# Performance work log

Hardware: AMD Instinct MI355X
Metric: run time of the kernel (lower is better)

The kernel has to match this reference:

```python
import jax, jax.numpy as jnp
import numpy as np

# physical / init constants (from DPINeuron.__init__ with default 1e-12 currents)
I0 = 5e-13
UT = 0.025
KAPPA = (0.75 + 0.66) / 2  # 0.705
CMEM, CAMPA, CSHUNT = 3e-12, 2e-12, 2e-12
ITAU_MEM = 1e-12
IGAIN_MEM = 1e-12
ITAU_AMPA = 1e-12
IGAIN_AMPA = 1e-12
ITH = 1e-12
IPFB_TH = 1e-12
IPFB_NORM = 1e-12
REFP = 0.0
DT = 0.001
TAU_MEM = UT / KAPPA * CMEM / ITAU_MEM
TAU_AMPA = UT / KAPPA * CAMPA / ITAU_AMPA
TAU_SHUNT = UT / KAPPA * CSHUNT / ITAU_AMPA
SLOPE = 25.0  # fast_sigmoid surrogate slope

@jax.custom_vjp
def ste_round(x):
    return jnp.round(x)

def _round_fwd(x):
    return jnp.round(x), None

def _round_bwd(_, g):
    return (g,)  # straight-through estimator

ste_round.defvjp(_round_fwd, _round_bwd)

@jax.custom_vjp
def fast_sigmoid(x):
    return (x > 0).astype(x.dtype)

def _fs_fwd(x):
    return (x > 0).astype(x.dtype), x

def _fs_bwd(x, g):
    return (g / (SLOPE * jnp.abs(x) + 1.0) ** 2,)

fast_sigmoid.defvjp(_fs_fwd, _fs_bwd)

B, N_IN, N_OUT = 4096, 2048, 2048

def setup_inputs() -> dict:
    key = jax.random.key(0)
    k1, = jax.random.split(key, 1)
    X = (jax.random.uniform(k1, (B, N_IN), dtype=jnp.float32) < 0.1).astype(jnp.float32)  # sparse input spikes
    return {
        "X": X,
        "W_ampa": jnp.ones((N_OUT, N_IN), jnp.float32),   # init.constant_(1.0)
        "W_shunt": jnp.ones((N_OUT, N_IN), jnp.float32),
        "Imem": jnp.full((B, N_OUT), I0, jnp.float32),    # initialize(): zeros + I0
        "Iampa": jnp.full((B, N_OUT), I0, jnp.float32),
        "Ishunt": jnp.full((B, N_OUT), I0, jnp.float32),
        "refractory": jnp.zeros((B, N_OUT), jnp.float32),
        "Idc": jnp.float32(1e-12),
        "Iw_ampa": jnp.float32(1e-12),
        "Iw_shunt": jnp.float32(1e-12),
        "alpha": jnp.float32(IGAIN_MEM / ITAU_MEM),       # 1.0
        "beta": jnp.float32(1.0 + I0 / ITAU_MEM),         # 1.5
    }

def reference(X, W_ampa, W_shunt, Imem, Iampa, Ishunt, refractory,
              Idc, Iw_ampa, Iw_shunt, alpha, beta):
    Iahp = I0
    Inmda = I0
    # synapse projections with STE-rounded weights: [B, n_out]
    numSynAmpa = jnp.einsum('bi,oi->bo', X, ste_round(W_ampa))
    numSynShunt = jnp.einsum('bi,oi->bo', X, ste_round(W_shunt))

    dIampa = -Iampa / TAU_AMPA
    Iampa = Iampa + (IGAIN_AMPA / ITAU_AMPA) * Iw_ampa * numSynAmpa
    dIshunt = -Ishunt / TAU_SHUNT
    Ishunt = Ishunt + (IGAIN_AMPA / ITAU_AMPA) * Iw_shunt * numSynShunt

    Iin = Idc + Iampa + Inmda - Ishunt
    Iin = Iin * (refractory <= 0)
    Iin = jnp.maximum(Iin, I0)

    Ifb = (I0 ** (1.0 / (KAPPA + 1.0))) * Imem ** (KAPPA / (KAPPA + 1.0)) \
          / (1.0 + jnp.exp(-IPFB_NORM * (Imem - IPFB_TH)))
    f_imem = Ifb / ITAU_MEM * (Imem + IGAIN_MEM)
    dImem = (alpha * (Iin - ITAU_MEM - Iahp) - beta * Imem
             + jax.lax.stop_gradient(f_imem)) / (TAU_MEM * (1.0 + IGAIN_MEM / Imem))
    Imem = jnp.maximum(Imem + dImem * DT, I0)

    # note: original code applies dIshunt decay to Iampa (kept faithful)
    Iampa = jnp.maximum(Iampa + dIampa * DT, I0)
    Iampa = jnp.maximum(Iampa + dIshunt * DT, I0)

    spike = fast_sigmoid(Imem - ITH)
    Imem = (1.0 - spike) * Imem + spike * I0
    refractory = jnp.maximum(refractory - DT, 0.0)
    refractory = (1.0 - spike) * refractory + spike * REFP
    return spike, Imem, Iampa, Ishunt, refractory
```

## Files before the change

### kernel.cpp

```cpp
#include <hip/hip_runtime.h>
#include <cmath>

#ifndef __has_builtin
#define __has_builtin(x) 0
#endif

#define B_DIM 4096
#define K_DIM 2048
#define N_DIM 2048

#define BM 128
#define BN 128
#define BK 64

typedef __attribute__((ext_vector_type(4))) float f32x4;
typedef __attribute__((ext_vector_type(4))) int i32x4;
typedef __attribute__((ext_vector_type(16))) signed char i8x16;


__device__ __forceinline__ signed char f2i8(float f) {
    int t = __float2int_rn(f);
    t = t < -127 ? -127 : (t > 127 ? 127 : t);
    return (signed char)t;
}

__device__ __forceinline__ void gl2lds16(const void* g, void* l) {
#if __has_builtin(__builtin_amdgcn_global_load_lds)
    __builtin_amdgcn_global_load_lds((__attribute__((address_space(1))) void*)g,
                                     (__attribute__((address_space(3))) void*)l,
                                     16, 0, 0);
#else
    *(uint4*)l = *(const uint4*)g;
#endif
}

#define VMWAIT_(n) asm volatile("s_waitcnt vmcnt(" #n ")" ::: "memory")
#define VMWAIT(n)  VMWAIT_(n)
#define FENCE      asm volatile("" ::: "memory")
#define SBARRIER   do { FENCE; __builtin_amdgcn_s_barrier(); FENCE; } while (0)


__global__ void cast_x_kernel(const float* __restrict__ X,
                              signed char* __restrict__ Xb) {
    size_t i = ((size_t)blockIdx.x * 256 + threadIdx.x) * 16;
    i8x16 o;
#pragma unroll
    for (int j = 0; j < 16; j += 4) {
        f32x4 a = *(const f32x4*)(X + i + j);
        o[j]     = f2i8(a[0]);
        o[j + 1] = f2i8(a[1]);
        o[j + 2] = f2i8(a[2]);
        o[j + 3] = f2i8(a[3]);
    }
    *(i8x16*)(Xb + i) = o;
}

__global__ void cast_w_kernel(const float* __restrict__ Wa,
                              const float* __restrict__ Ws,
                              signed char* __restrict__ Wab,
                              signed char* __restrict__ Wsb) {
    size_t i = ((size_t)blockIdx.x * 256 + threadIdx.x) * 16;
    i8x16 oa, os;
#pragma unroll
    for (int j = 0; j < 16; j += 4) {
        f32x4 a = *(const f32x4*)(Wa + i + j);
        f32x4 s = *(const f32x4*)(Ws + i + j);
        oa[j]     = f2i8(a[0]); oa[j + 1] = f2i8(a[1]);
        oa[j + 2] = f2i8(a[2]); oa[j + 3] = f2i8(a[3]);
        os[j]     = f2i8(s[0]); os[j + 1] = f2i8(s[1]);
        os[j + 2] = f2i8(s[2]); os[j + 3] = f2i8(s[3]);
    }
    *(i8x16*)(Wab + i) = oa;
    *(i8x16*)(Wsb + i) = os;
}


#define RS 132

__device__ __forceinline__ void stage_tile(int tt, int bufIdx, int tid, int m0, int n0,
                                           unsigned char* smem,
                                           const signed char* __restrict__ Xb,
                                           const signed char* __restrict__ Wab,
                                           const signed char* __restrict__ Wsb) {
    unsigned char* bb = smem + bufIdx * 24576;
    const int k0s = tt * BK;
#pragma unroll
    for (int j = 0; j < 2; j++) {
        const int c   = j * 256 + tid;
        const int row = c >> 2;
        const int js  = (c & 3) ^ ((row >> 1) & 3);
        gl2lds16(Xb + (size_t)(m0 + row) * K_DIM + k0s + js * 16, bb + c * 16);
    }
#pragma unroll
    for (int j = 0; j < 2; j++) {
        const int c   = j * 256 + tid;
        const int row = c >> 2;
        const int js  = (c & 3) ^ ((row >> 1) & 3);
        const size_t go = (size_t)(n0 + row) * K_DIM + k0s + js * 16;
        gl2lds16(Wab + go, bb + 8192  + c * 16);
        gl2lds16(Wsb + go, bb + 16384 + c * 16);
    }
}

#define TILE_STEP(t_, rb_, sb_, WAITN, DOSTG)                                 \
{                                                                             \
  VMWAIT(WAITN); SBARRIER;                                                    \
  const unsigned char* bb = smem + (rb_) * 24576;                             \
  const signed char* sA  = (const signed char*)bb;                            \
  const signed char* sWa = (const signed char*)(bb + 8192);                   \
  const signed char* sWs = (const signed char*)(bb + 16384);                  \
  i32x4 af[4], ba[4], bs[4];                                                  \
  _Pragma("unroll") for (int mi = 0; mi < 4; mi++)                            \
      af[mi] = *(const i32x4*)(sA + (wm + mi * 16 + frow) * 64 + slot16);     \
  _Pragma("unroll") for (int ni = 0; ni < 4; ni++) {                          \
      const int o = (wn + ni * 16 + frow) * 64 + slot16;                      \
      ba[ni] = *(const i32x4*)(sWa + o);                                      \
      bs[ni] = *(const i32x4*)(sWs + o);                                      \
  }                                                                           \
  if (DOSTG) stage_tile((t_) + 2, (sb_), tid, m0, n0, smem, Xb, Wab, Wsb);    \
  __builtin_amdgcn_sched_barrier(0);                                          \
  _Pragma("unroll") for (int mi = 0; mi < 4; mi++)                            \
  _Pragma("unroll") for (int ni = 0; ni < 4; ni++) {                          \
      accA[mi][ni] = __builtin_amdgcn_mfma_i32_16x16x64_i8(af[mi], ba[ni], accA[mi][ni], 0, 0, 0); \
      accS[mi][ni] = __builtin_amdgcn_mfma_i32_16x16x64_i8(af[mi], bs[ni], accS[mi][ni], 0, 0, 0); \
  }                                                                           \
}

__global__ __launch_bounds__(256, 2)
void dpi_fused_kernel(const signed char* __restrict__ Xb,
                      const signed char* __restrict__ Wab,
                      const signed char* __restrict__ Wsb,
                      const float* __restrict__ gImem,
                      const float* __restrict__ gIampa,
                      const float* __restrict__ gIshunt,
                      const float* __restrict__ gRefr,
                      const float* __restrict__ pIdc,
                      const float* __restrict__ pIwa,
                      const float* __restrict__ pIws,
                      const float* __restrict__ pAlpha,
                      const float* __restrict__ pBeta,
                      float* __restrict__ out,
                      float i0pow, float kexp, float tau_mem, float inv_tau_syn)
{
    __shared__ __align__(16) unsigned char smem[73728];
    float* na_buf = (float*)smem;
    float* ns_buf = (float*)(smem + 16896);

    const int tid  = threadIdx.x;
    const int lane = tid & 63;
    const int wave = tid >> 6;

    const int lin = blockIdx.x;
    const int xcd = lin & 7;
    const int loc = lin >> 3;
    const int mb  = (xcd & 3) * 8 + (loc & 7);
    const int nb  = (xcd >> 2) * 8 + (loc >> 3);
    const int m0  = mb * BM;
    const int n0  = nb * BN;

    const int wm = (wave & 1) * 64;
    const int wn = (wave >> 1) * 64;

    i32x4 accA[4][4], accS[4][4];
#pragma unroll
    for (int i = 0; i < 4; i++)
#pragma unroll
        for (int j = 0; j < 4; j++) { accA[i][j] = (i32x4)0; accS[i][j] = (i32x4)0; }

    const int frow   = lane & 15;
    const int kq     = lane >> 4;
    const int slot16 = (kq ^ ((frow >> 1) & 3)) * 16;

    stage_tile(0, 0, tid, m0, n0, smem, Xb, Wab, Wsb); FENCE;
    stage_tile(1, 1, tid, m0, n0, smem, Xb, Wab, Wsb); FENCE;

    for (int tb = 0; tb < 30; tb += 3) {
        TILE_STEP(tb + 0, 0, 2, 6, 1);
        TILE_STEP(tb + 1, 1, 0, 6, 1);
        TILE_STEP(tb + 2, 2, 1, 6, 1);
    }
    TILE_STEP(30, 0, 2, 6, 0);
    TILE_STEP(31, 1, 0, 0, 0);

    SBARRIER;

    const float idc   = *pIdc;
    const float iwa   = *pIwa;
    const float iws   = *pIws;
    const float alpha = *pAlpha;
    const float beta  = *pBeta;

    const size_t plane = (size_t)B_DIM * N_DIM;
    float* __restrict__ oSpike = out;
    float* __restrict__ oImem  = out + plane;
    float* __restrict__ oIampa = out + 2 * plane;
    float* __restrict__ oIsh   = out + 3 * plane;
    float* __restrict__ oRefr  = out + 4 * plane;

    const int rowgroup = wm >> 6;
    const int quad4    = (lane >> 4) << 2;
    const int cseg     = (tid & 31) * 4;
    const int rgrp     = tid >> 5;

#pragma unroll
    for (int s = 0; s < 4; s++) {
#pragma unroll
        for (int ni = 0; ni < 4; ni++) {
            const int lcol = wn + ni * 16 + (lane & 15);
#pragma unroll
            for (int r = 0; r < 4; r++) {
                const int lrow = rowgroup * 16 + quad4 + r;
                na_buf[lrow * RS + lcol] = (float)accA[s][ni][r];
                ns_buf[lrow * RS + lcol] = (float)accS[s][ni][r];
            }
        }
        __syncthreads();

#pragma unroll
        for (int q = 0; q < 4; q++) {
            const int lrow = rgrp * 4 + q;
            const int grow = m0 + (lrow >> 4) * 64 + s * 16 + (lrow & 15);
            const size_t idx = (size_t)grow * N_DIM + n0 + cseg;

            const f32x4 na4 = *(const f32x4*)(na_buf + lrow * RS + cseg);
            const f32x4 ns4 = *(const f32x4*)(ns_buf + lrow * RS + cseg);
            const f32x4 im4 = *(const f32x4*)(gImem   + idx);
            const f32x4 ia4 = *(const f32x4*)(gIampa  + idx);
            const f32x4 is4 = *(const f32x4*)(gIshunt + idx);
            const f32x4 rf4 = *(const f32x4*)(gRefr   + idx);

            f32x4 sp_o, im_o, ia_o, is_o, rf_o;
#pragma unroll
            for (int e = 0; e < 4; e++) {
                const float na  = na4[e];
                const float ns  = ns4[e];
                const float im  = im4[e];
                const float ia  = ia4[e];
                const float ish = is4[e];
                const float rf  = rf4[e];

                const float dIampa  = -ia * inv_tau_syn;
                const float ia2     = ia + iwa * na;
                const float dIshunt = -ish * inv_tau_syn;
                const float ish2    = ish + iws * ns;

                float Iin = idc + ia2 + 5e-13f - ish2;
                Iin = (rf <= 0.0f) ? Iin : 0.0f;
                Iin = fmaxf(Iin, 5e-13f);

                const float ifb = i0pow *
                    __builtin_amdgcn_exp2f(kexp * __builtin_amdgcn_logf(im)) * 0.5f;
                const float fimem = ifb * 1e12f * (im + 1e-12f);
                const float dImem = (alpha * ((Iin - 1e-12f) - 5e-13f) - beta * im + fimem)
                                    / (tau_mem * (1.0f + 1e-12f / im));
                float im2 = fmaxf(im + dImem * 0.001f, 5e-13f);

                float ia3 = fmaxf(ia2 + dIampa * 0.001f, 5e-13f);
                ia3       = fmaxf(ia3 + dIshunt * 0.001f, 5e-13f);

                const float spike = (im2 - 1e-12f > 0.0f) ? 1.0f : 0.0f;
                im2 = (spike > 0.0f) ? 5e-13f : im2;
                float rf2 = fmaxf(rf - 0.001f, 0.0f);
                rf2 = (spike > 0.0f) ? 0.0f : rf2;

                sp_o[e] = spike; im_o[e] = im2; ia_o[e] = ia3;
                is_o[e] = ish2;  rf_o[e] = rf2;
            }

            *(f32x4*)(oSpike + idx) = sp_o;
            *(f32x4*)(oImem  + idx) = im_o;
            *(f32x4*)(oIampa + idx) = ia_o;
            *(f32x4*)(oIsh   + idx) = is_o;
            *(f32x4*)(oRefr  + idx) = rf_o;
        }
        __syncthreads();
    }
}


extern "C" void kernel_launch(void* const* d_in, const int* in_sizes, int n_in,
                              void* d_out, int out_size, void* d_ws, size_t ws_size,
                              hipStream_t stream) {
    (void)in_sizes; (void)n_in; (void)out_size; (void)ws_size;

    const float* X       = (const float*)d_in[0];
    const float* W_ampa  = (const float*)d_in[1];
    const float* W_shunt = (const float*)d_in[2];
    const float* Imem    = (const float*)d_in[3];
    const float* Iampa   = (const float*)d_in[4];
    const float* Ishunt  = (const float*)d_in[5];
    const float* Refr    = (const float*)d_in[6];
    const float* pIdc    = (const float*)d_in[7];
    const float* pIwa    = (const float*)d_in[8];
    const float* pIws    = (const float*)d_in[9];
    const float* pAlpha  = (const float*)d_in[10];
    const float* pBeta   = (const float*)d_in[11];

    signed char* Xb  = (signed char*)d_ws;
    signed char* Wab = Xb  + (size_t)B_DIM * K_DIM;
    signed char* Wsb = Wab + (size_t)N_DIM * K_DIM;

    const float i0pow       = (float)std::pow(5e-13, 1.0 / 1.705);
    const float kexp        = (float)(0.705 / 1.705);
    const float tau_mem     = (float)(0.025 / 0.705 * 3.0);
    const float inv_tau_syn = (float)(1.0 / (0.025 / 0.705 * 2.0));

    cast_x_kernel<<<dim3((B_DIM * K_DIM) / (256 * 16)), dim3(256), 0, stream>>>(X, Xb);
    cast_w_kernel<<<dim3((N_DIM * K_DIM) / (256 * 16)), dim3(256), 0, stream>>>(
        W_ampa, W_shunt, Wab, Wsb);

    dpi_fused_kernel<<<dim3(512), dim3(256), 0, stream>>>(
        Xb, Wab, Wsb, Imem, Iampa, Ishunt, Refr,
        pIdc, pIwa, pIws, pAlpha, pBeta,
        (float*)d_out, i0pow, kexp, tau_mem, inv_tau_syn);
}
```

Baseline: 364.7 us.

## Merge cast kernels, reorder staging, raise MFMA priority, prefetch epilogue state

Merges the two int8 cast kernels into one launch. Moves the next-tile async staging before the LDS fragment reads and wraps the MFMA block in s_setprio so matrix work gets issue priority. In the epilogue it issues the global state loads for half the rows before the barrier, hiding their latency behind the LDS write/sync, and replaces __syncthreads with an explicit lgkmcnt wait plus barrier. Several small scheduling ideas combined; the staging reorder could add LDS/VMEM contention in the main loop.

```diff
diff --git a/kernel.cpp b/kernel.cpp
--- a/kernel.cpp
+++ b/kernel.cpp
@@ -36,42 +36,46 @@
 
 #define VMWAIT_(n) asm volatile("s_waitcnt vmcnt(" #n ")" ::: "memory")
 #define VMWAIT(n)  VMWAIT_(n)
+#define LGKM0      asm volatile("s_waitcnt lgkmcnt(0)" ::: "memory")
 #define FENCE      asm volatile("" ::: "memory")
 #define SBARRIER   do { FENCE; __builtin_amdgcn_s_barrier(); FENCE; } while (0)
-
-
-__global__ void cast_x_kernel(const float* __restrict__ X,
-                              signed char* __restrict__ Xb) {
-    size_t i = ((size_t)blockIdx.x * 256 + threadIdx.x) * 16;
-    i8x16 o;
-#pragma unroll
-    for (int j = 0; j < 16; j += 4) {
-        f32x4 a = *(const f32x4*)(X + i + j);
-        o[j]     = f2i8(a[0]);
-        o[j + 1] = f2i8(a[1]);
-        o[j + 2] = f2i8(a[2]);
-        o[j + 3] = f2i8(a[3]);
-    }
-    *(i8x16*)(Xb + i) = o;
-}
-
-__global__ void cast_w_kernel(const float* __restrict__ Wa,
-                              const float* __restrict__ Ws,
-                              signed char* __restrict__ Wab,
-                              signed char* __restrict__ Wsb) {
-    size_t i = ((size_t)blockIdx.x * 256 + threadIdx.x) * 16;
-    i8x16 oa, os;
-#pragma unroll
-    for (int j = 0; j < 16; j += 4) {
-        f32x4 a = *(const f32x4*)(Wa + i + j);
-        f32x4 s = *(const f32x4*)(Ws + i + j);
-        oa[j]     = f2i8(a[0]); oa[j + 1] = f2i8(a[1]);
-        oa[j + 2] = f2i8(a[2]); oa[j + 3] = f2i8(a[3]);
-        os[j]     = f2i8(s[0]); os[j + 1] = f2i8(s[1]);
-        os[j + 2] = f2i8(s[2]); os[j + 3] = f2i8(s[3]);
-    }
-    *(i8x16*)(Wab + i) = oa;
-    *(i8x16*)(Wsb + i) = os;
+#define LDSBARRIER do { LGKM0; SBARRIER; } while (0)
+
+
+__global__ void cast_all_kernel(const float* __restrict__ X,
+                                const float* __restrict__ Wa,
+                                const float* __restrict__ Ws,
+                                signed char* __restrict__ Xb,
+                                signed char* __restrict__ Wab,
+                                signed char* __restrict__ Wsb) {
+    const int bid = blockIdx.x;
+    if (bid < 2048) {
+        size_t i = ((size_t)bid * 256 + threadIdx.x) * 16;
+        i8x16 o;
+#pragma unroll
+        for (int j = 0; j < 16; j += 4) {
+            f32x4 a = *(const f32x4*)(X + i + j);
+            o[j]     = f2i8(a[0]);
+            o[j + 1] = f2i8(a[1]);
+            o[j + 2] = f2i8(a[2]);
+            o[j + 3] = f2i8(a[3]);
+        }
+        *(i8x16*)(Xb + i) = o;
+    } else {
+        size_t i = ((size_t)(bid - 2048) * 256 + threadIdx.x) * 16;
+        i8x16 oa, os;
+#pragma unroll
+        for (int j = 0; j < 16; j += 4) {
+            f32x4 a = *(const f32x4*)(Wa + i + j);
+            f32x4 s = *(const f32x4*)(Ws + i + j);
+            oa[j]     = f2i8(a[0]); oa[j + 1] = f2i8(a[1]);
+            oa[j + 2] = f2i8(a[2]); oa[j + 3] = f2i8(a[3]);
+            os[j]     = f2i8(s[0]); os[j + 1] = f2i8(s[1]);
+            os[j + 2] = f2i8(s[2]); os[j + 3] = f2i8(s[3]);
+        }
+        *(i8x16*)(Wab + i) = oa;
+        *(i8x16*)(Wsb + i) = os;
+    }
 }
 
 
@@ -105,6 +109,7 @@
 #define TILE_STEP(t_, rb_, sb_, WAITN, DOSTG)                                 \
 {                                                                             \
   VMWAIT(WAITN); SBARRIER;                                                    \
+  if (DOSTG) stage_tile((t_) + 2, (sb_), tid, m0, n0, smem, Xb, Wab, Wsb);    \
   const unsigned char* bb = smem + (rb_) * 24576;                             \
   const signed char* sA  = (const signed char*)bb;                            \
   const signed char* sWa = (const signed char*)(bb + 8192);                   \
@@ -117,13 +122,14 @@
       ba[ni] = *(const i32x4*)(sWa + o);                                      \
       bs[ni] = *(const i32x4*)(sWs + o);                                      \
   }                                                                           \
-  if (DOSTG) stage_tile((t_) + 2, (sb_), tid, m0, n0, smem, Xb, Wab, Wsb);    \
   __builtin_amdgcn_sched_barrier(0);                                          \
+  __builtin_amdgcn_s_setprio(1);                                              \
   _Pragma("unroll") for (int mi = 0; mi < 4; mi++)                            \
   _Pragma("unroll") for (int ni = 0; ni < 4; ni++) {                          \
       accA[mi][ni] = __builtin_amdgcn_mfma_i32_16x16x64_i8(af[mi], ba[ni], accA[mi][ni], 0, 0, 0); \
       accS[mi][ni] = __builtin_amdgcn_mfma_i32_16x16x64_i8(af[mi], bs[ni], accS[mi][ni], 0, 0, 0); \
   }                                                                           \
+  __builtin_amdgcn_s_setprio(0);                                              \
 }
 
 __global__ __launch_bounds__(256, 2)
@@ -214,7 +220,20 @@
                 ns_buf[lrow * RS + lcol] = (float)accS[s][ni][r];
             }
         }
-        __syncthreads();
+
+        f32x4 p_im[2], p_ia[2], p_is[2], p_rf[2];
+#pragma unroll
+        for (int q = 0; q < 2; q++) {
+            const int lrow = rgrp * 4 + q;
+            const int grow = m0 + (lrow >> 4) * 64 + s * 16 + (lrow & 15);
+            const size_t idx = (size_t)grow * N_DIM + n0 + cseg;
+            p_im[q] = *(const f32x4*)(gImem   + idx);
+            p_ia[q] = *(const f32x4*)(gIampa  + idx);
+            p_is[q] = *(const f32x4*)(gIshunt + idx);
+            p_rf[q] = *(const f32x4*)(gRefr   + idx);
+        }
+
+        LDSBARRIER;
 
 #pragma unroll
         for (int q = 0; q < 4; q++) {
@@ -224,10 +243,15 @@
 
             const f32x4 na4 = *(const f32x4*)(na_buf + lrow * RS + cseg);
             const f32x4 ns4 = *(const f32x4*)(ns_buf + lrow * RS + cseg);
-            const f32x4 im4 = *(const f32x4*)(gImem   + idx);
-            const f32x4 ia4 = *(const f32x4*)(gIampa  + idx);
-            const f32x4 is4 = *(const f32x4*)(gIshunt + idx);
-            const f32x4 rf4 = *(const f32x4*)(gRefr   + idx);
+            f32x4 im4, ia4, is4, rf4;
+            if (q < 2) {
+                im4 = p_im[q]; ia4 = p_ia[q]; is4 = p_is[q]; rf4 = p_rf[q];
+            } else {
+                im4 = *(const f32x4*)(gImem   + idx);
+                ia4 = *(const f32x4*)(gIampa  + idx);
+                is4 = *(const f32x4*)(gIshunt + idx);
+                rf4 = *(const f32x4*)(gRefr   + idx);
+            }
 
             f32x4 sp_o, im_o, ia_o, is_o, rf_o;
 #pragma unroll
@@ -273,7 +297,8 @@
             *(f32x4*)(oIsh   + idx) = is_o;
             *(f32x4*)(oRefr  + idx) = rf_o;
         }
-        __syncthreads();
+
+        LDSBARRIER;
     }
 }
 
@@ -305,9 +330,8 @@
     const float tau_mem     = (float)(0.025 / 0.705 * 3.0);
     const float inv_tau_syn = (float)(1.0 / (0.025 / 0.705 * 2.0));
 
-    cast_x_kernel<<<dim3((B_DIM * K_DIM) / (256 * 16)), dim3(256), 0, stream>>>(X, Xb);
-    cast_w_kernel<<<dim3((N_DIM * K_DIM) / (256 * 16)), dim3(256), 0, stream>>>(
-        W_ampa, W_shunt, Wab, Wsb);
+    cast_all_kernel<<<dim3(3072), dim3(256), 0, stream>>>(
+        X, W_ampa, W_shunt, Xb, Wab, Wsb);
 
     dpi_fused_kernel<<<dim3(512), dim3(256), 0, stream>>>(
         Xb, Wab, Wsb, Imem, Iampa, Ishunt, Refr,
```

Result: no change. 360.4 us (-1.2%).
